# Kernel optimization log

Hardware: AMD Instinct MI355X
Metric: run time of the kernel (lower is better)

The kernel has to match this reference:

```python
import jax, jax.numpy as jnp
import numpy as np

# Dims: C = 8*8*4 = 256 input channels, O = 8*8*8 = 512 output channels,
# space_rank = 4, TT ranks = (4, 16, 16).

def setup_inputs() -> dict:
    key = jax.random.key(0)
    ks = jax.random.split(key, 6)
    inp = jax.random.normal(ks[0], (32, 256, 32, 32), dtype=jnp.float32)
    # space_factor: (space_rank, 1, kH, kW)
    space_factor = jax.random.normal(ks[1], (4, 1, 3, 3), dtype=jnp.float32) * 0.3
    # factors[i]: (in_i, rank_i, rank_{i+1}, out_i)
    factor0 = jax.random.normal(ks[2], (8, 4, 16, 8), dtype=jnp.float32) * 0.1
    factor1 = jax.random.normal(ks[3], (8, 16, 16, 8), dtype=jnp.float32) * 0.08
    # last_factor: (in_last, rank_last, out_last)
    last_factor = jax.random.normal(ks[4], (4, 16, 8), dtype=jnp.float32) * 0.1
    bias = jax.random.uniform(ks[5], (512,), dtype=jnp.float32, minval=-0.02, maxval=0.02)
    return {"input": inp, "space_factor": space_factor, "factor0": factor0,
            "factor1": factor1, "last_factor": last_factor, "bias": bias}


def reference(input, space_factor, factor0, factor1, last_factor, bias):
    B, C, H, W = input.shape
    sr = space_factor.shape[0]
    # Depthwise conv: each of the C channels convolved with the same
    # `space_rank` filters (torch repeat along out-channel dim + groups=C).
    w = jnp.tile(space_factor, (C, 1, 1, 1))  # (C*sr, 1, kH, kW)
    y = jax.lax.conv_general_dilated(
        input, w, window_strides=(1, 1), padding=[(1, 1), (1, 1)],
        feature_group_count=C,
        dimension_numbers=("NCHW", "OIHW", "NCHW"))  # (B, C*sr, H', W')
    Hp, Wp = y.shape[2], y.shape[3]
    # (B, n0, n1, n2, sr, H', W') with (n0,n1,n2) = input_chanel_shape
    t = y.reshape(B, 8, 8, 4, sr, Hp, Wp)
    # Contract the tiny TT cores first (optimal order found by tn.contractors.optimal):
    # chain: (n0, n1, n2, r0, o0, o1, o2) -- only ~0.5M elements.
    chain = jnp.einsum("apqx,bqry,crz->abcpxyz", factor0, factor1, last_factor)
    # One big contraction over (n0, n1, n2, r0): effectively a GEMM
    # (B*H'*W', C*sr) x (C*sr, O).
    out = jnp.einsum("nabcphw,abcpxyz->nxyzhw", t, chain)
    out = out.reshape(B, 512, Hp, Wp)
    return out + bias[None, :, None, None]
```

## Files before the change

kernel.cpp:

```cpp
#include <hip/hip_runtime.h>

typedef unsigned short ushort_t;
typedef __attribute__((ext_vector_type(8))) short bf16x8;
typedef __attribute__((ext_vector_type(8))) unsigned short ushort8;
typedef __attribute__((ext_vector_type(4))) float f32x4;

__device__ __forceinline__ unsigned short f2bf(float f) {
  union { float f; unsigned u; } x; x.f = f;
  unsigned r = x.u + 0x7FFFu + ((x.u >> 16) & 1u);
  return (unsigned short)(r >> 16);
}

__global__ void chain_g_kernel(const float* __restrict__ f1,
                               const float* __restrict__ lf,
                               float* __restrict__ g) {
  int idx = blockIdx.x * 256 + threadIdx.x;
  int z = idx & 7, c = (idx >> 3) & 3, y = (idx >> 5) & 7,
      q = (idx >> 8) & 15, b = idx >> 12;
  float s = 0.f;
  #pragma unroll
  for (int r = 0; r < 16; ++r)
    s += f1[((b * 16 + q) * 16 + r) * 8 + y] * lf[(c * 16 + r) * 8 + z];
  g[idx] = s;
}

__global__ void chain_kernel(const float* __restrict__ f0,
                             const float* __restrict__ g,
                             ushort_t* __restrict__ chainT) {
  int idx = blockIdx.x * 256 + threadIdx.x;
  int k = idx & 1023, o = idx >> 10;
  int p = k & 3, c = (k >> 2) & 3, b = (k >> 4) & 7, a = k >> 7;
  int z = o & 7, y = (o >> 3) & 7, x = o >> 6;
  float s = 0.f;
  #pragma unroll
  for (int q = 0; q < 16; ++q)
    s += f0[((a * 4 + p) * 16 + q) * 8 + x] *
         g[(((b * 16 + q) * 8 + y) * 4 + c) * 8 + z];
  chainT[idx] = f2bf(s);
}

__global__ __launch_bounds__(256) void conv_kernel(const float* __restrict__ in,
                                                   const float* __restrict__ sf,
                                                   ushort_t* __restrict__ t) {
  __shared__ float in_lds[64][244];
  __shared__ float sf_l[36];
  int bid = blockIdx.x;
  int cq = bid & 3, h4 = (bid >> 2) & 7, n = bid >> 5;
  int h0 = h4 * 4;
  int tid = threadIdx.x;
  if (tid < 36) sf_l[tid] = sf[tid];
  for (int e = tid; e < 384; e += 256) {
    int ch = e / 6, r = e % 6;
    in_lds[ch][r * 40 + 3] = 0.f;
    in_lds[ch][r * 40 + 36] = 0.f;
  }
  const float* inb = in + ((size_t)n * 256 + cq * 64) * 1024;
  #pragma unroll
  for (int i = 0; i < 12; ++i) {
    int e = tid + i * 256;
    int ch = e / 48, rem = e % 48;
    int r = rem >> 3, w4 = rem & 7;
    int hh = h0 - 1 + r;
    float4 v = make_float4(0.f, 0.f, 0.f, 0.f);
    if (hh >= 0 && hh < 32)
      v = *(const float4*)&inb[(size_t)ch * 1024 + hh * 32 + w4 * 4];
    *(float4*)&in_lds[ch][r * 40 + 4 + w4 * 4] = v;
  }
  __syncthreads();
  float sfr[36];
  #pragma unroll
  for (int i = 0; i < 36; ++i) sfr[i] = sf_l[i];
  int w = tid >> 3, gg = tid & 7;
  size_t m0 = (size_t)n * 1024 + (size_t)h0 * 32 + w;
  #pragma unroll
  for (int j = 0; j < 4; ++j) {
    float acc[4][2][4];
    #pragma unroll
    for (int b = 0; b < 2; ++b) {
      int ch = j * 16 + gg * 2 + b;
      float vals[6][3];
      #pragma unroll
      for (int r = 0; r < 6; ++r)
        #pragma unroll
        for (int dw = 0; dw < 3; ++dw)
          vals[r][dw] = in_lds[ch][r * 40 + 3 + w + dw];
      #pragma unroll
      for (int hh = 0; hh < 4; ++hh)
        #pragma unroll
        for (int p = 0; p < 4; ++p) {
          float s = 0.f;
          #pragma unroll
          for (int dr = 0; dr < 3; ++dr)
            #pragma unroll
            for (int dw = 0; dw < 3; ++dw)
              s += vals[hh + dr][dw] * sfr[p * 9 + dr * 3 + dw];
          acc[hh][b][p] = s;
        }
    }
    #pragma unroll
    for (int hh = 0; hh < 4; ++hh) {
      ushort8 outv;
      #pragma unroll
      for (int b = 0; b < 2; ++b)
        #pragma unroll
        for (int p = 0; p < 4; ++p) outv[b * 4 + p] = f2bf(acc[hh][b][p]);
      *(ushort8*)&t[(m0 + hh * 32) * 1024 + (size_t)(cq * 256 + j * 64 + gg * 8)] = outv;
    }
  }
}

#define AS1 __attribute__((address_space(1)))
#define AS3 __attribute__((address_space(3)))
#define BARRIER  __builtin_amdgcn_s_barrier()
#define LGKMCNT0 asm volatile("s_waitcnt lgkmcnt(0)" ::: "memory")
#define VMCNT4   asm volatile("s_waitcnt vmcnt(4)" ::: "memory")
#define VMCNT0   asm volatile("s_waitcnt vmcnt(0)" ::: "memory")

__global__ __launch_bounds__(512, 2) void gemm_kernel(const ushort_t* __restrict__ tA,
                                                      const ushort_t* __restrict__ tB,
                                                      const float* __restrict__ bias,
                                                      float* __restrict__ out) {
  __shared__ __align__(16) ushort_t smem[65536];
  int tid = threadIdx.x;
  int bid = blockIdx.x;
  int wg = (bid & 7) * 32 + (bid >> 3);
  int tile_m = (wg >> 1) * 256;
  int tile_n = (wg & 1) * 256;

  int lane = tid & 63, wv = tid >> 6;
  int wm2 = wv >> 2, wn4 = wv & 3;
  int lr = lane & 15, kg = lane >> 4;
  int kph0 = ((kg * 8) ^ ((lane & 7) * 8));
  int kph1 = ((32 + kg * 8) ^ ((lane & 7) * 8));
  int arow = wm2 * 128 + lr;
  int brow = wn4 * 64 + lr;

  int srow = tid >> 3;
  int scol = ((tid & 7) ^ (srow & 7)) * 8;
  const ushort_t* sA = tA + (size_t)(tile_m + srow) * 1024 + scol;
  const ushort_t* sB = tB + (size_t)(tile_n + srow) * 1024 + scol;

#define STAGE_A(buf, koff, h)                                                                  \
  __builtin_amdgcn_global_load_lds((const AS1 void*)(sA + (size_t)((h)*128) * 1024 + (koff)),  \
      (AS3 void*)&smem[(buf)*16384 + (h)*8192 + tid*8], 16, 0, 0);                             \
  __builtin_amdgcn_global_load_lds((const AS1 void*)(sA + (size_t)((h)*128+64) * 1024 + (koff)),\
      (AS3 void*)&smem[(buf)*16384 + (h)*8192 + 4096 + tid*8], 16, 0, 0);
#define STAGE_B(buf, koff, h)                                                                  \
  __builtin_amdgcn_global_load_lds((const AS1 void*)(sB + (size_t)((h)*128) * 1024 + (koff)),  \
      (AS3 void*)&smem[32768 + (buf)*16384 + (h)*8192 + tid*8], 16, 0, 0);                     \
  __builtin_amdgcn_global_load_lds((const AS1 void*)(sB + (size_t)((h)*128+64) * 1024 + (koff)),\
      (AS3 void*)&smem[32768 + (buf)*16384 + (h)*8192 + 4096 + tid*8], 16, 0, 0);

#define READ_A(dst, mbase, buf)                                                                \
  _Pragma("unroll")                                                                            \
  for (int mf = 0; mf < 4; ++mf) {                                                             \
    dst[mf][0] = *(const bf16x8*)&smem[(buf)*16384 + (arow + (mbase) + mf*16)*64 + kph0];      \
    dst[mf][1] = *(const bf16x8*)&smem[(buf)*16384 + (arow + (mbase) + mf*16)*64 + kph1];      \
  }
#define READ_B(dst, nbase, buf)                                                                \
  _Pragma("unroll")                                                                            \
  for (int nf = 0; nf < 2; ++nf) {                                                             \
    dst[nf][0] = *(const bf16x8*)&smem[32768 + (buf)*16384 + (brow + (nbase) + nf*16)*64 + kph0];\
    dst[nf][1] = *(const bf16x8*)&smem[32768 + (buf)*16384 + (brow + (nbase) + nf*16)*64 + kph1];\
  }
#define Q_MFMA(AF, BF, MB, NB)                                                                 \
  __builtin_amdgcn_s_setprio(1);                                                              \
  _Pragma("unroll")                                                                            \
  for (int mf = 0; mf < 4; ++mf)                                                               \
    _Pragma("unroll")                                                                          \
    for (int nf = 0; nf < 2; ++nf)                                                             \
      _Pragma("unroll")                                                                        \
      for (int ks = 0; ks < 2; ++ks)                                                           \
        acc[(MB) + mf][(NB) + nf] = __builtin_amdgcn_mfma_f32_16x16x32_bf16(                   \
            AF[mf][ks], BF[nf][ks], acc[(MB) + mf][(NB) + nf], 0, 0, 0);                       \
  __builtin_amdgcn_s_setprio(0);

  f32x4 acc[8][4];
  #pragma unroll
  for (int i = 0; i < 8; ++i)
    #pragma unroll
    for (int j = 0; j < 4; ++j) acc[i][j] = (f32x4){0.f, 0.f, 0.f, 0.f};

  bf16x8 a1[4][2], a2[4][2], b1[2][2], b2[2][2];

  STAGE_A(0, 0, 0) STAGE_A(0, 0, 1) STAGE_B(0, 0, 0) STAGE_B(0, 0, 1)
  STAGE_A(1, 64, 0) STAGE_A(1, 64, 1)
  VMCNT4; BARRIER;

#define ITER(I_, FULL)                                                                         \
  {                                                                                            \
    int k1 = (2*(I_)+1)*64, k2 = (2*(I_)+2)*64, k3 = (2*(I_)+3)*64;                            \
                            \
    READ_A(a1, 0, 0) READ_A(a2, 64, 0) READ_B(b1, 0, 0)                                        \
    STAGE_B(1, k1, 0) BARRIER; LGKMCNT0;                                                       \
    Q_MFMA(a1, b1, 0, 0) BARRIER;                                                              \
                                                                                       \
    READ_B(b2, 32, 0) STAGE_B(1, k1, 1) BARRIER; LGKMCNT0;                                     \
    Q_MFMA(a1, b2, 0, 2) BARRIER;                                                              \
                                                                                       \
    if (FULL) { STAGE_A(0, k2, 0) } BARRIER;                                                   \
    Q_MFMA(a2, b2, 4, 2) BARRIER;                                                              \
                         \
    if (FULL) { STAGE_A(0, k2, 1) } BARRIER;                                                   \
    Q_MFMA(a2, b1, 4, 0)                                                                       \
    if (FULL) { VMCNT4; } else { VMCNT0; }                                                     \
    BARRIER;                                                                                   \
                                                                       \
    READ_A(a1, 0, 1) READ_A(a2, 64, 1) READ_B(b1, 0, 1)                                        \
    if (FULL) { STAGE_B(0, k2, 0) } BARRIER; LGKMCNT0;                                         \
    Q_MFMA(a1, b1, 0, 0) BARRIER;                                                              \
                                                                                       \
    READ_B(b2, 32, 1) if (FULL) { STAGE_B(0, k2, 1) } BARRIER; LGKMCNT0;                       \
    Q_MFMA(a1, b2, 0, 2) BARRIER;                                                              \
                                                                                       \
    if (FULL) { STAGE_A(1, k3, 0) } BARRIER;                                                   \
    Q_MFMA(a2, b2, 4, 2) BARRIER;                                                              \
                                     \
    if (FULL) { STAGE_A(1, k3, 1) } BARRIER;                                                   \
    Q_MFMA(a2, b1, 4, 0)                                                                       \
    if (FULL) { VMCNT4; }                                                                      \
    BARRIER;                                                                                   \
  }

  for (int I = 0; I < 7; ++I) ITER(I, 1)
  ITER(7, 0)
#undef ITER

  #pragma unroll
  for (int mf = 0; mf < 8; ++mf)
    #pragma unroll
    for (int nf = 0; nf < 4; ++nf) {
      int m = tile_m + wm2 * 128 + mf * 16 + kg * 4;
      int o = tile_n + wn4 * 64 + nf * 16 + lr;
      float bv = bias[o];
      f32x4 v = acc[mf][nf];
      v[0] += bv; v[1] += bv; v[2] += bv; v[3] += bv;
      *(f32x4*)&out[(size_t)(m >> 10) * 524288 + (size_t)o * 1024 + (size_t)(m & 1023)] = v;
    }
}

extern "C" void kernel_launch(void* const* d_in, const int* in_sizes, int n_in,
                              void* d_out, int out_size, void* d_ws, size_t ws_size,
                              hipStream_t stream) {
  (void)in_sizes; (void)n_in; (void)out_size; (void)ws_size;
  const float* in   = (const float*)d_in[0];
  const float* sf   = (const float*)d_in[1];
  const float* f0   = (const float*)d_in[2];
  const float* f1   = (const float*)d_in[3];
  const float* lf   = (const float*)d_in[4];
  const float* bias = (const float*)d_in[5];
  float* out = (float*)d_out;

  char* ws = (char*)d_ws;
  ushort_t* t      = (ushort_t*)ws;
  ushort_t* chainT = (ushort_t*)(ws + 67108864);
  float*    g      = (float*)(ws + 67108864 + 1048576);

  hipLaunchKernelGGL(chain_g_kernel, dim3(128),  dim3(256), 0, stream, f1, lf, g);
  hipLaunchKernelGGL(chain_kernel,   dim3(2048), dim3(256), 0, stream, f0, g, chainT);
  hipLaunchKernelGGL(conv_kernel,    dim3(1024), dim3(256), 0, stream, in, sf, t);
  hipLaunchKernelGGL(gemm_kernel,    dim3(256),  dim3(512), 0, stream, t, chainT, bias, out);
}
```

Before: 80.38 us.

## Fuse TT chain kernels via shared memory and interleave GEMM LDS reads

```diff
diff --git a/kernel.cpp b/kernel.cpp
--- a/kernel.cpp
+++ b/kernel.cpp
@@ -11,32 +11,35 @@
   return (unsigned short)(r >> 16);
 }
 
-__global__ void chain_g_kernel(const float* __restrict__ f1,
-                               const float* __restrict__ lf,
-                               float* __restrict__ g) {
-  int idx = blockIdx.x * 256 + threadIdx.x;
-  int z = idx & 7, c = (idx >> 3) & 3, y = (idx >> 5) & 7,
-      q = (idx >> 8) & 15, b = idx >> 12;
-  float s = 0.f;
-  #pragma unroll
-  for (int r = 0; r < 16; ++r)
-    s += f1[((b * 16 + q) * 16 + r) * 8 + y] * lf[(c * 16 + r) * 8 + z];
-  g[idx] = s;
-}
-
-__global__ void chain_kernel(const float* __restrict__ f0,
-                             const float* __restrict__ g,
-                             ushort_t* __restrict__ chainT) {
-  int idx = blockIdx.x * 256 + threadIdx.x;
-  int k = idx & 1023, o = idx >> 10;
-  int p = k & 3, c = (k >> 2) & 3, b = (k >> 4) & 7, a = k >> 7;
+__global__ __launch_bounds__(256) void chain_kernel(const float* __restrict__ f0,
+                                                    const float* __restrict__ f1,
+                                                    const float* __restrict__ lf,
+                                                    ushort_t* __restrict__ chainT) {
+  __shared__ float gs[512];
+  int o = blockIdx.x;
   int z = o & 7, y = (o >> 3) & 7, x = o >> 6;
-  float s = 0.f;
-  #pragma unroll
-  for (int q = 0; q < 16; ++q)
-    s += f0[((a * 4 + p) * 16 + q) * 8 + x] *
-         g[(((b * 16 + q) * 8 + y) * 4 + c) * 8 + z];
-  chainT[idx] = f2bf(s);
+  int tid = threadIdx.x;
+  #pragma unroll
+  for (int i = 0; i < 2; ++i) {
+    int e = tid + i * 256;
+    int c = e & 3, q = (e >> 2) & 15, b = e >> 6;
+    float s = 0.f;
+    #pragma unroll
+    for (int r = 0; r < 16; ++r)
+      s += f1[((b * 16 + q) * 16 + r) * 8 + y] * lf[(c * 16 + r) * 8 + z];
+    gs[e] = s;
+  }
+  __syncthreads();
+  #pragma unroll
+  for (int j = 0; j < 4; ++j) {
+    int k = tid + j * 256;
+    int p = k & 3, c = (k >> 2) & 3, b = (k >> 4) & 7, a = k >> 7;
+    float s = 0.f;
+    #pragma unroll
+    for (int q = 0; q < 16; ++q)
+      s += f0[((a * 4 + p) * 16 + q) * 8 + x] * gs[(b * 16 + q) * 4 + c];
+    chainT[(size_t)o * 1024 + k] = f2bf(s);
+  }
 }
 
 __global__ __launch_bounds__(256) void conv_kernel(const float* __restrict__ in,
@@ -190,32 +193,33 @@
 #define ITER(I_, FULL)                                                                         \
   {                                                                                            \
     int k1 = (2*(I_)+1)*64, k2 = (2*(I_)+2)*64, k3 = (2*(I_)+3)*64;                            \
-                            \
-    READ_A(a1, 0, 0) READ_A(a2, 64, 0) READ_B(b1, 0, 0)                                        \
+                             \
+    READ_A(a1, 0, 0) READ_B(b1, 0, 0)                                                          \
     STAGE_B(1, k1, 0) BARRIER; LGKMCNT0;                                                       \
     Q_MFMA(a1, b1, 0, 0) BARRIER;                                                              \
-                                                                                       \
-    READ_B(b2, 32, 0) STAGE_B(1, k1, 1) BARRIER; LGKMCNT0;                                     \
+                      \
+    READ_B(b2, 32, 0) READ_A(a2, 64, 0) STAGE_B(1, k1, 1) BARRIER; LGKMCNT0;                   \
     Q_MFMA(a1, b2, 0, 2) BARRIER;                                                              \
-                                                                                       \
+                                           \
     if (FULL) { STAGE_A(0, k2, 0) } BARRIER;                                                   \
     Q_MFMA(a2, b2, 4, 2) BARRIER;                                                              \
-                         \
+                                                           \
     if (FULL) { STAGE_A(0, k2, 1) } BARRIER;                                                   \
     Q_MFMA(a2, b1, 4, 0)                                                                       \
     if (FULL) { VMCNT4; } else { VMCNT0; }                                                     \
     BARRIER;                                                                                   \
-                                                                       \
-    READ_A(a1, 0, 1) READ_A(a2, 64, 1) READ_B(b1, 0, 1)                                        \
+                                                                                       \
+    READ_A(a1, 0, 1) READ_B(b1, 0, 1)                                                          \
     if (FULL) { STAGE_B(0, k2, 0) } BARRIER; LGKMCNT0;                                         \
     Q_MFMA(a1, b1, 0, 0) BARRIER;                                                              \
                                                                                        \
-    READ_B(b2, 32, 1) if (FULL) { STAGE_B(0, k2, 1) } BARRIER; LGKMCNT0;                       \
+    READ_B(b2, 32, 1) READ_A(a2, 64, 1)                                                        \
+    if (FULL) { STAGE_B(0, k2, 1) } BARRIER; LGKMCNT0;                                         \
     Q_MFMA(a1, b2, 0, 2) BARRIER;                                                              \
                                                                                        \
     if (FULL) { STAGE_A(1, k3, 0) } BARRIER;                                                   \
     Q_MFMA(a2, b2, 4, 2) BARRIER;                                                              \
-                                     \
+                                                 \
     if (FULL) { STAGE_A(1, k3, 1) } BARRIER;                                                   \
     Q_MFMA(a2, b1, 4, 0)                                                                       \
     if (FULL) { VMCNT4; }                                                                      \
@@ -254,10 +258,8 @@
   char* ws = (char*)d_ws;
   ushort_t* t      = (ushort_t*)ws;
   ushort_t* chainT = (ushort_t*)(ws + 67108864);
-  float*    g      = (float*)(ws + 67108864 + 1048576);
-
-  hipLaunchKernelGGL(chain_g_kernel, dim3(128),  dim3(256), 0, stream, f1, lf, g);
-  hipLaunchKernelGGL(chain_kernel,   dim3(2048), dim3(256), 0, stream, f0, g, chainT);
-  hipLaunchKernelGGL(conv_kernel,    dim3(1024), dim3(256), 0, stream, in, sf, t);
-  hipLaunchKernelGGL(gemm_kernel,    dim3(256),  dim3(512), 0, stream, t, chainT, bias, out);
-}
+
+  hipLaunchKernelGGL(chain_kernel, dim3(512),  dim3(256), 0, stream, f0, f1, lf, chainT);
+  hipLaunchKernelGGL(conv_kernel,  dim3(1024), dim3(256), 0, stream, in, sf, t);
+  hipLaunchKernelGGL(gemm_kernel,  dim3(256),  dim3(512), 0, stream, t, chainT, bias, out);
+}
```

Result: faster. 76.91 us (-4.3%).
